# Performance work log

Hardware: AMD Instinct MI355X
Metric: run time of the kernel (lower is better)

Reference implementation:

```python
import jax, jax.numpy as jnp
import numpy as np

BS, C, H, W = 16, 64, 128, 128
NC = 80          # num classes (hardcoded 80 in original via expand(-1, 80, -1))
TOPK = 128
TAU = 0.07
EPS = 1e-12      # F.normalize eps


def setup_inputs() -> dict:
    key = jax.random.key(0)
    k1, k2, k3, k4 = jax.random.split(key, 4)
    feat = jax.random.normal(k1, (BS, C, H, W), dtype=jnp.float32)
    score = jax.random.uniform(k2, (BS, NC, H, W), dtype=jnp.float32)
    # hm: GT heatmap with exactly one 1.0 peak per (batch, class) for ~half the classes
    pos = jax.random.randint(k3, (BS, NC), 0, H * W)
    present = jax.random.bernoulli(k4, 0.5, (BS, NC)).astype(jnp.float32)
    b = jnp.arange(BS)[:, None]
    c = jnp.arange(NC)[None, :]
    hm = jnp.zeros((BS, NC, H * W), jnp.float32).at[b, c, pos].set(present)
    hm = hm.reshape(BS, NC, H, W)
    return {"feat": feat, "score": score, "hm": hm}


def reference(feat, score, hm):
    bs, c, h, w = feat.shape
    nc = hm.shape[1]
    hw = h * w
    score = jax.lax.stop_gradient(score)  # score.detach()

    # F.normalize(feat, dim=1)
    feat = feat / jnp.maximum(jnp.linalg.norm(feat, axis=1, keepdims=True), EPS)

    # q: feature at the hm==1 peak of each present class (one peak per (b,cls))
    peak = (hm == 1.0).astype(feat.dtype)                       # [bs,nc,h,w]
    q = jnp.einsum('bnhw,bchw->bnc', peak, feat)                # [bs,nc,c]
    class_mask = (peak.sum(axis=(2, 3)) > 0).astype(feat.dtype)  # [bs,nc]

    # k0: hm-weighted pooled feature per class, L2-normalized
    k0 = jnp.einsum('bchw,bnhw->bnc', feat, hm)                 # [bs,nc,c]
    k0 = k0 / jnp.maximum(jnp.linalg.norm(k0, axis=-1, keepdims=True), EPS)

    # mask score: zero at GT locations and for absent classes
    hm_free = (hm.sum(axis=1) == 0).astype(score.dtype)         # [bs,h,w]
    score = score * hm_free[:, None] * class_mask[:, :, None, None]

    max_values = score.max(axis=1).reshape(bs, hw)              # [bs,hw]
    class_indices = score.argmax(axis=1).reshape(bs, hw)        # [bs,hw]
    topk_values, topk_indices = jax.lax.top_k(max_values, TOPK)  # [bs,topk]
    k_all_mask_t = (topk_values > 0).astype(feat.dtype)         # [bs,topk]
    topk_class = jnp.take_along_axis(class_indices, topk_indices, axis=1)  # [bs,topk]

    feat_flat = feat.reshape(bs, c, hw)
    k_top = jnp.take_along_axis(feat_flat, topk_indices[:, None, :], axis=2)  # [bs,c,topk]
    k_top = k_top.transpose(0, 2, 1)                            # [bs,topk,c]

    # pseudo heatmap: 0.9 at selected (class, pos) pairs with positive score
    b_idx = jnp.arange(bs)[:, None]
    pseudo_hm = jnp.zeros((bs, nc, hw), feat.dtype).at[
        b_idx, topk_class, topk_indices].set(k_all_mask_t * 0.9)
    pseudo_hm = pseudo_hm.reshape(bs, nc, h, w)

    # positive mask: selected positions whose pseudo class matches the query class
    class_ids = jnp.arange(nc, dtype=feat.dtype)
    target = jnp.where(class_mask[:, :, None] == 1, class_ids[None, :, None], -1.0)  # [bs,nc,1]
    k_mask_top = (target == topk_class[:, None, :].astype(feat.dtype)).astype(feat.dtype)
    k_mask_top = k_mask_top * k_all_mask_t[:, None, :]          # [bs,nc,topk]
    k0_mask = class_mask[:, :, None] * jnp.eye(nc, dtype=feat.dtype)  # [bs,nc,nc]

    k_all = jnp.concatenate([k_top, k0], axis=1)                # [bs,topk+nc,c]
    k_mask = jnp.concatenate([k_mask_top, k0_mask], axis=-1)    # [bs,nc,topk+nc]
    k_all_mask = jnp.concatenate([k_all_mask_t, class_mask], axis=-1)  # [bs,topk+nc]

    sim = jnp.exp(jnp.einsum('bnc,bkc->bnk', q, k_all) / TAU)   # [bs,nc,topk+nc]
    sim_sum = (sim * k_all_mask[:, None, :]).sum(-1, keepdims=True)
    sim_sum = jnp.where(sim_sum == 0, 1.0, sim_sum)
    logit = jnp.where(k_mask > 0, sim / sim_sum, 1.0)
    log_loss = (jnp.log(logit) * k_mask).sum(-1)                # [bs,nc]
    num = k_mask.sum(-1)
    num = jnp.where(num == 0, 1.0, num)
    count = class_mask.sum()
    loss = ((log_loss / num) * class_mask).sum() / count
    return (-loss, pseudo_hm)
```

## Files before the change

### kernel.cpp

```cpp
#include <hip/hip_runtime.h>
#include <math.h>

#define BS 16
#define C 64
#define H 128
#define W 128
#define HW (H*W)
#define NC 80
#define TOPK 128
#define KALL (TOPK+NC)
#define TAU 0.07f
#define EPSN 1e-12f
#define OUT_N 20971521
#define ZBLK 1280

__global__ __launch_bounds__(1024) void k_peak_zero(const float* __restrict__ hm,
                                                    int* __restrict__ peak_pos,
                                                    float* __restrict__ out) {
    int t = threadIdx.x;
    if (blockIdx.x >= BS * NC) {
        int zb = blockIdx.x - BS * NC;
        float4* o4 = (float4*)out;
        float4 z = make_float4(0.f, 0.f, 0.f, 0.f);
        int idx = zb * 1024 + t;
        #pragma unroll
        for (int j = 0; j < 4; ++j) o4[idx + j * (ZBLK * 1024)] = z;
        if (zb == 0 && t == 0) out[OUT_N - 1] = 0.0f;
        return;
    }
    __shared__ int wmax[16];
    int bn = blockIdx.x;
    int lane = t & 63, wid = t >> 6;
    const float4* p = (const float4*)(hm + (size_t)bn * HW);
    int found = -1;
    #pragma unroll
    for (int j = 0; j < 4; ++j) {
        int gi = j * 1024 + t;
        float4 v = p[gi];
        int base = gi * 4;
        if (v.x == 1.0f) found = base;
        if (v.y == 1.0f) found = base + 1;
        if (v.z == 1.0f) found = base + 2;
        if (v.w == 1.0f) found = base + 3;
    }
    #pragma unroll
    for (int off = 1; off < 64; off <<= 1) found = max(found, __shfl_xor(found, off));
    if (lane == 0) wmax[wid] = found;
    __syncthreads();
    if (t == 0) {
        int m = wmax[0];
        #pragma unroll
        for (int i = 1; i < 16; ++i) m = max(m, wmax[i]);
        peak_pos[bn] = m;
    }
}

__global__ void k_max(const float* __restrict__ score, const int* __restrict__ peak_pos,
                      float* __restrict__ maxv, int* __restrict__ clsidx) {
    __shared__ int pk[NC];
    int b = blockIdx.y;
    int g = blockIdx.x * blockDim.x + threadIdx.x;
    if (threadIdx.x < NC) pk[threadIdx.x] = peak_pos[b * NC + threadIdx.x];
    __syncthreads();
    const float4* sb = (const float4*)(score + (size_t)b * NC * HW);
    int p0 = g * 4;
    int pp0 = pk[0];
    float m0 = (pp0 >= 0) ? 1.0f : 0.0f;
    float4 v0 = sb[g];
    float bx = v0.x * m0, by = v0.y * m0, bz = v0.z * m0, bw = v0.w * m0;
    int ix = 0, iy = 0, iz = 0, iw = 0;
    bool pe0 = (pp0 == p0), pe1 = (pp0 == p0 + 1), pe2 = (pp0 == p0 + 2), pe3 = (pp0 == p0 + 3);
    #pragma unroll 8
    for (int n = 1; n < NC; ++n) {
        int pp = pk[n];
        float m = (pp >= 0) ? 1.0f : 0.0f;
        float4 v = sb[(size_t)n * (HW / 4) + g];
        float vx = v.x * m, vy = v.y * m, vz = v.z * m, vw = v.w * m;
        if (vx > bx) { bx = vx; ix = n; }
        if (vy > by) { by = vy; iy = n; }
        if (vz > bz) { bz = vz; iz = n; }
        if (vw > bw) { bw = vw; iw = n; }
        pe0 |= (pp == p0); pe1 |= (pp == p0 + 1); pe2 |= (pp == p0 + 2); pe3 |= (pp == p0 + 3);
    }
    if (pe0) { bx = 0.0f; ix = 0; }
    if (pe1) { by = 0.0f; iy = 0; }
    if (pe2) { bz = 0.0f; iz = 0; }
    if (pe3) { bw = 0.0f; iw = 0; }
    ((float4*)maxv)[(size_t)b * (HW / 4) + g] = make_float4(bx, by, bz, bw);
    ((int4*)clsidx)[(size_t)b * (HW / 4) + g] = make_int4(ix, iy, iz, iw);
}

__global__ __launch_bounds__(1024) void k_topk(const float* __restrict__ maxv,
                                               const int* __restrict__ clsidx,
                                               float* __restrict__ topkv,
                                               int* __restrict__ topki,
                                               int* __restrict__ topkc) {
    __shared__ unsigned int hist[2048];
    __shared__ unsigned int wtot[16];
    __shared__ unsigned int woff[16];
    __shared__ unsigned int s_pref;
    __shared__ int s_rank;
    __shared__ unsigned int s_bin;
    __shared__ unsigned int s_above;

    int b = blockIdx.x, t = threadIdx.x;
    int lane = t & 63, wid = t >> 6;
    unsigned int key[16];
    const float4* mv4 = (const float4*)(maxv + (size_t)b * HW);
    #pragma unroll
    for (int j4 = 0; j4 < 4; ++j4) {
        float4 v = mv4[t * 4 + j4];
        key[j4 * 4 + 0] = __float_as_uint(v.x);
        key[j4 * 4 + 1] = __float_as_uint(v.y);
        key[j4 * 4 + 2] = __float_as_uint(v.z);
        key[j4 * 4 + 3] = __float_as_uint(v.w);
    }

    if (t == 0) { s_pref = 0u; s_rank = TOPK; }

    const int shifts[3] = {21, 10, 0};
    const int widths[3] = {11, 11, 10};

    for (int rnd = 0; rnd < 3; ++rnd) {
        int sh = shifts[rnd], w = widths[rnd];
        unsigned mask = (1u << w) - 1u;
        hist[t] = 0u; hist[t + 1024] = 0u;
        __syncthreads();
        unsigned pref = s_pref;
        int hiShift = sh + w;
        #pragma unroll
        for (int j = 0; j < 16; ++j) {
            unsigned k = key[j];
            bool ok = (rnd == 0) || ((k >> hiShift) == pref);
            if (ok) atomicAdd(&hist[(k >> sh) & mask], 1u);
        }
        __syncthreads();
        unsigned p = hist[2 * t] + hist[2 * t + 1];
        unsigned s = p;
        #pragma unroll
        for (int off = 1; off < 64; off <<= 1) {
            unsigned o = __shfl_down(s, off);
            if (lane + off < 64) s += o;
        }
        if (lane == 0) wtot[wid] = s;
        __syncthreads();
        if (wid == 0) {
            unsigned vv = (lane < 16) ? wtot[lane] : 0u;
            unsigned ss = vv;
            #pragma unroll
            for (int off = 1; off < 64; off <<= 1) {
                unsigned o = __shfl_down(ss, off);
                if (lane + off < 64) ss += o;
            }
            if (lane < 16) woff[lane] = ss - vv;
        }
        __syncthreads();
        unsigned S_t = s + woff[wid];
        unsigned S_next = S_t - p;
        int r = s_rank;
        if ((int)S_t >= r && (int)S_next < r) {
            unsigned hi = hist[2 * t + 1];
            if ((int)(S_next + hi) >= r) { s_bin = 2u * t + 1u; s_above = S_next; }
            else                         { s_bin = 2u * t;      s_above = S_next + hi; }
        }
        __syncthreads();
        if (t == 0) {
            s_pref = (s_pref << w) | s_bin;
            s_rank = s_rank - (int)s_above;
        }
        __syncthreads();
    }
    unsigned K = s_pref;
    int need_eq = s_rank;
    int cnt_gt = TOPK - need_eq;

    int cg = 0, ce = 0;
    #pragma unroll
    for (int j = 0; j < 16; ++j) { cg += (key[j] > K); ce += (key[j] == K); }
    unsigned v = ((unsigned)cg << 16) | (unsigned)ce;
    unsigned sc = v;
    #pragma unroll
    for (int off = 1; off < 64; off <<= 1) {
        unsigned o = __shfl_up(sc, off);
        if (lane >= off) sc += o;
    }
    if (lane == 63) wtot[wid] = sc;
    __syncthreads();
    if (wid == 0) {
        unsigned vv = (lane < 16) ? wtot[lane] : 0u;
        unsigned ss = vv;
        #pragma unroll
        for (int off = 1; off < 64; off <<= 1) {
            unsigned o = __shfl_up(ss, off);
            if (lane >= off) ss += o;
        }
        if (lane < 16) woff[lane] = ss - vv;
    }
    __syncthreads();
    unsigned ex = (sc - v) + woff[wid];
    int pg = (int)(ex >> 16);
    int pe = (int)(ex & 0xffffu);
    int lg = 0, le = 0;
    #pragma unroll
    for (int j = 0; j < 16; ++j) {
        unsigned k = key[j];
        int slot = -1;
        if (k > K) { slot = pg + lg; ++lg; }
        else if (k == K) { int er = pe + le; ++le; if (er < need_eq) slot = cnt_gt + er; }
        if (slot >= 0) {
            int idx = t * 16 + j;
            topkv[b * TOPK + slot] = __uint_as_float(k);
            topki[b * TOPK + slot] = idx;
            topkc[b * TOPK + slot] = clsidx[(size_t)b * HW + idx];
        }
    }
}

__global__ void k_gather(const float* __restrict__ feat, const int* __restrict__ peak_pos,
                         const int* __restrict__ topki, float* k_all, float* qv) {
    int bk = blockIdx.x;
    int b = bk / KALL, k = bk % KALL, c = threadIdx.x;
    int pos;
    if (k < TOPK) {
        pos = topki[b * TOPK + k];
    } else {
        int n = k - TOPK;
        int pp = peak_pos[b * NC + n];
        if (pp < 0) {
            k_all[((size_t)b * KALL + k) * C + c] = 0.0f;
            qv[((size_t)b * NC + n) * C + c] = 0.0f;
            return;
        }
        pos = pp;
    }
    float v = feat[((size_t)b * C + c) * HW + pos];
    float ss = v * v;
    #pragma unroll
    for (int off = 1; off < 64; off <<= 1) ss += __shfl_xor(ss, off);
    float qc = v / fmaxf(sqrtf(ss), EPSN);
    if (k < TOPK) {
        k_all[((size_t)b * KALL + k) * C + c] = qc;
    } else {
        int n = k - TOPK;
        qv[((size_t)b * NC + n) * C + c] = qc;
        float qq = qc * qc;
        #pragma unroll
        for (int off = 1; off < 64; off <<= 1) qq += __shfl_xor(qq, off);
        k_all[((size_t)b * KALL + k) * C + c] = qc / fmaxf(sqrtf(qq), EPSN);
    }
}

__global__ void k_loss(const float* __restrict__ k_all, const float* __restrict__ qv,
                       const int* __restrict__ peak_pos, const float* __restrict__ topkv,
                       const int* __restrict__ topkc, float* loss_bn) {
    __shared__ float qs[C];
    __shared__ float r1[256];
    __shared__ float r2[256];
    __shared__ float s_simsum, s_num;
    int bn = blockIdx.x;
    int b = bn / NC, n = bn % NC, t = threadIdx.x;
    if (peak_pos[bn] < 0) { if (t == 0) loss_bn[bn] = 0.0f; return; }
    if (t < C) qs[t] = qv[(size_t)bn * C + t];
    __syncthreads();
    float sim = 0.0f, kam = 0.0f, km = 0.0f;
    if (t < KALL) {
        const float* kr = k_all + ((size_t)b * KALL + t) * C;
        float dot = 0.0f;
        for (int c2 = 0; c2 < C; ++c2) dot += qs[c2] * kr[c2];
        sim = expf(dot / TAU);
        if (t < TOPK) {
            float posm = (topkv[b * TOPK + t] > 0.0f) ? 1.0f : 0.0f;
            kam = posm;
            km = (topkc[b * TOPK + t] == n) ? posm : 0.0f;
        } else {
            int j = t - TOPK;
            kam = (peak_pos[b * NC + j] >= 0) ? 1.0f : 0.0f;
            km = (j == n) ? 1.0f : 0.0f;
        }
    }
    r1[t] = sim * kam;
    r2[t] = km;
    __syncthreads();
    for (int s = 128; s > 0; s >>= 1) {
        if (t < s) { r1[t] += r1[t + s]; r2[t] += r2[t + s]; }
        __syncthreads();
    }
    if (t == 0) {
        float ss = r1[0];
        s_simsum = (ss == 0.0f) ? 1.0f : ss;
        s_num = (r2[0] == 0.0f) ? 1.0f : r2[0];
    }
    __syncthreads();
    r1[t] = (km > 0.0f) ? logf(sim / s_simsum) : 0.0f;
    __syncthreads();
    for (int s = 128; s > 0; s >>= 1) {
        if (t < s) r1[t] += r1[t + s];
        __syncthreads();
    }
    if (t == 0) loss_bn[bn] = r1[0] / s_num;
}

__global__ void k_scatter_final(const float* __restrict__ topkv, const int* __restrict__ topki,
                                const int* __restrict__ topkc,
                                const float* __restrict__ loss_bn,
                                const int* __restrict__ peak_pos, float* out) {
    if (blockIdx.x < 8) {
        int i = blockIdx.x * 256 + threadIdx.x;
        int b = i / TOPK;
        if (topkv[i] > 0.0f)
            out[1 + ((size_t)b * NC + topkc[i]) * HW + topki[i]] = 0.9f;
        return;
    }
    __shared__ float r1[256];
    __shared__ float r2[256];
    int t = threadIdx.x;
    float s = 0.0f, cnt = 0.0f;
    for (int i = t; i < BS * NC; i += 256) {
        s += loss_bn[i];
        cnt += (peak_pos[i] >= 0) ? 1.0f : 0.0f;
    }
    r1[t] = s; r2[t] = cnt;
    __syncthreads();
    for (int st = 128; st > 0; st >>= 1) {
        if (t < st) { r1[t] += r1[t + st]; r2[t] += r2[t + st]; }
        __syncthreads();
    }
    if (t == 0) out[0] = -(r1[0] / r2[0]);
}

extern "C" void kernel_launch(void* const* d_in, const int* in_sizes, int n_in,
                              void* d_out, int out_size, void* d_ws, size_t ws_size,
                              hipStream_t stream) {
    const float* feat  = (const float*)d_in[0];
    const float* score = (const float*)d_in[1];
    const float* hm    = (const float*)d_in[2];
    float* out = (float*)d_out;

    char* ws = (char*)d_ws;
    size_t off = 0;
    auto alloc = [&](size_t bytes) -> void* {
        void* p = ws + off;
        off += (bytes + 255) & ~(size_t)255;
        return p;
    };
    int*   peak_pos = (int*)  alloc((size_t)BS * NC * 4);
    float* maxv     = (float*)alloc((size_t)BS * HW * 4);
    int*   clsidx   = (int*)  alloc((size_t)BS * HW * 4);
    float* topkv    = (float*)alloc((size_t)BS * TOPK * 4);
    int*   topki    = (int*)  alloc((size_t)BS * TOPK * 4);
    int*   topkc    = (int*)  alloc((size_t)BS * TOPK * 4);
    float* k_all    = (float*)alloc((size_t)BS * KALL * C * 4);
    float* qv       = (float*)alloc((size_t)BS * NC * C * 4);
    float* loss_bn  = (float*)alloc((size_t)BS * NC * 4);

    k_peak_zero<<<BS * NC + ZBLK, 1024, 0, stream>>>(hm, peak_pos, out);
    dim3 gmax(HW / 4 / 256, BS);
    k_max<<<gmax, 256, 0, stream>>>(score, peak_pos, maxv, clsidx);
    k_topk<<<BS, 1024, 0, stream>>>(maxv, clsidx, topkv, topki, topkc);
    k_gather<<<BS * KALL, 64, 0, stream>>>(feat, peak_pos, topki, k_all, qv);
    k_loss<<<BS * NC, 256, 0, stream>>>(k_all, qv, peak_pos, topkv, topkc, loss_bn);
    k_scatter_final<<<9, 256, 0, stream>>>(topkv, topki, topkc, loss_bn, peak_pos, out);
}
```

Baseline: 93.48 us.

## Split output zeroing across first three kernels and fuse scatter into gather

The zero-fill of the large pseudo-heatmap output is split into three chunks. Extra blocks carrying those chunks are appended to the peak, max and top-k kernels, so the memset overlaps with the underutilized top-k and peak phases instead of running all at once in the first kernel. The 0.9 scatter moves into an extra block of the gather kernel, which now packs four rows per 256-thread block. The final reduction becomes a single-block kernel. This relies on the scatter running after all zeroing, which stream order still guarantees.

```diff
diff --git a/kernel.cpp b/kernel.cpp
--- a/kernel.cpp
+++ b/kernel.cpp
@@ -12,30 +12,32 @@
 #define TAU 0.07f
 #define EPSN 1e-12f
 #define OUT_N 20971521
-#define ZBLK 1280
-
-__global__ __launch_bounds__(1024) void k_peak_zero(const float* __restrict__ hm,
-                                                    int* __restrict__ peak_pos,
-                                                    float* __restrict__ out) {
+#define GBLK (BS*KALL/4)
+#define Z1BLK 1024
+#define Z2BLK 1024
+#define Z3BLK 256
+
+__global__ __launch_bounds__(256) void k_peak_z(const float* __restrict__ hm,
+                                                int* __restrict__ peak_pos,
+                                                float* __restrict__ out) {
     int t = threadIdx.x;
     if (blockIdx.x >= BS * NC) {
         int zb = blockIdx.x - BS * NC;
         float4* o4 = (float4*)out;
         float4 z = make_float4(0.f, 0.f, 0.f, 0.f);
-        int idx = zb * 1024 + t;
-        #pragma unroll
-        for (int j = 0; j < 4; ++j) o4[idx + j * (ZBLK * 1024)] = z;
-        if (zb == 0 && t == 0) out[OUT_N - 1] = 0.0f;
+        int base = zb * 2048;
+        #pragma unroll
+        for (int j = 0; j < 8; ++j) o4[base + j * 256 + t] = z;
         return;
     }
-    __shared__ int wmax[16];
+    __shared__ int wmax[4];
     int bn = blockIdx.x;
     int lane = t & 63, wid = t >> 6;
     const float4* p = (const float4*)(hm + (size_t)bn * HW);
     int found = -1;
     #pragma unroll
-    for (int j = 0; j < 4; ++j) {
-        int gi = j * 1024 + t;
+    for (int j = 0; j < 16; ++j) {
+        int gi = j * 256 + t;
         float4 v = p[gi];
         int base = gi * 4;
         if (v.x == 1.0f) found = base;
@@ -48,19 +50,30 @@
     if (lane == 0) wmax[wid] = found;
     __syncthreads();
     if (t == 0) {
-        int m = wmax[0];
-        #pragma unroll
-        for (int i = 1; i < 16; ++i) m = max(m, wmax[i]);
+        int m = max(max(wmax[0], wmax[1]), max(wmax[2], wmax[3]));
         peak_pos[bn] = m;
     }
 }
 
-__global__ void k_max(const float* __restrict__ score, const int* __restrict__ peak_pos,
-                      float* __restrict__ maxv, int* __restrict__ clsidx) {
+__global__ __launch_bounds__(256) void k_max_z(const float* __restrict__ score,
+                                               const int* __restrict__ peak_pos,
+                                               float* __restrict__ maxv,
+                                               int* __restrict__ clsidx,
+                                               float* __restrict__ out) {
+    int t = threadIdx.x;
+    if (blockIdx.x >= 256) {
+        int zb = blockIdx.x - 256;
+        float4* o4 = (float4*)out;
+        float4 z = make_float4(0.f, 0.f, 0.f, 0.f);
+        int base = 2097152 + zb * 2048;
+        #pragma unroll
+        for (int j = 0; j < 8; ++j) o4[base + j * 256 + t] = z;
+        return;
+    }
     __shared__ int pk[NC];
-    int b = blockIdx.y;
-    int g = blockIdx.x * blockDim.x + threadIdx.x;
-    if (threadIdx.x < NC) pk[threadIdx.x] = peak_pos[b * NC + threadIdx.x];
+    int b = blockIdx.x >> 4;
+    int g = (blockIdx.x & 15) * 256 + t;
+    if (t < NC) pk[t] = peak_pos[b * NC + t];
     __syncthreads();
     const float4* sb = (const float4*)(score + (size_t)b * NC * HW);
     int p0 = g * 4;
@@ -90,11 +103,23 @@
     ((int4*)clsidx)[(size_t)b * (HW / 4) + g] = make_int4(ix, iy, iz, iw);
 }
 
-__global__ __launch_bounds__(1024) void k_topk(const float* __restrict__ maxv,
-                                               const int* __restrict__ clsidx,
-                                               float* __restrict__ topkv,
-                                               int* __restrict__ topki,
-                                               int* __restrict__ topkc) {
+__global__ __launch_bounds__(1024) void k_topk_z(const float* __restrict__ maxv,
+                                                 const int* __restrict__ clsidx,
+                                                 float* __restrict__ topkv,
+                                                 int* __restrict__ topki,
+                                                 int* __restrict__ topkc,
+                                                 float* __restrict__ out) {
+    int t = threadIdx.x;
+    if (blockIdx.x >= BS) {
+        int zb = blockIdx.x - BS;
+        float4* o4 = (float4*)out;
+        float4 z = make_float4(0.f, 0.f, 0.f, 0.f);
+        int base = 4194304 + zb * 4096;
+        #pragma unroll
+        for (int j = 0; j < 4; ++j) o4[base + j * 1024 + t] = z;
+        if (zb == 0 && t == 0) out[OUT_N - 1] = 0.0f;
+        return;
+    }
     __shared__ unsigned int hist[2048];
     __shared__ unsigned int wtot[16];
     __shared__ unsigned int woff[16];
@@ -103,8 +128,9 @@
     __shared__ unsigned int s_bin;
     __shared__ unsigned int s_above;
 
-    int b = blockIdx.x, t = threadIdx.x;
+    int b = blockIdx.x;
     int lane = t & 63, wid = t >> 6;
+
     unsigned int key[16];
     const float4* mv4 = (const float4*)(maxv + (size_t)b * HW);
     #pragma unroll
@@ -216,10 +242,29 @@
     }
 }
 
-__global__ void k_gather(const float* __restrict__ feat, const int* __restrict__ peak_pos,
-                         const int* __restrict__ topki, float* k_all, float* qv) {
-    int bk = blockIdx.x;
-    int b = bk / KALL, k = bk % KALL, c = threadIdx.x;
+__global__ __launch_bounds__(256) void k_gather_sc(const float* __restrict__ feat,
+                                                   const int* __restrict__ peak_pos,
+                                                   const float* __restrict__ topkv,
+                                                   const int* __restrict__ topki,
+                                                   const int* __restrict__ topkc,
+                                                   float* __restrict__ k_all,
+                                                   float* __restrict__ qv,
+                                                   float* __restrict__ out) {
+    int t = threadIdx.x;
+    if (blockIdx.x == GBLK) {
+        #pragma unroll
+        for (int j = 0; j < 8; ++j) {
+            int i = j * 256 + t;
+            if (topkv[i] > 0.0f) {
+                int b = i >> 7;
+                out[1 + (((size_t)b * NC + topkc[i]) << 14) + topki[i]] = 0.9f;
+            }
+        }
+        return;
+    }
+    int wid = t >> 6, lane = t & 63;
+    int bk = blockIdx.x * 4 + wid;
+    int b = bk / KALL, k = bk % KALL, c = lane;
     int pos;
     if (k < TOPK) {
         pos = topki[b * TOPK + k];
@@ -250,9 +295,12 @@
     }
 }
 
-__global__ void k_loss(const float* __restrict__ k_all, const float* __restrict__ qv,
-                       const int* __restrict__ peak_pos, const float* __restrict__ topkv,
-                       const int* __restrict__ topkc, float* loss_bn) {
+__global__ __launch_bounds__(256) void k_loss(const float* __restrict__ k_all,
+                                              const float* __restrict__ qv,
+                                              const int* __restrict__ peak_pos,
+                                              const float* __restrict__ topkv,
+                                              const int* __restrict__ topkc,
+                                              float* __restrict__ loss_bn) {
     __shared__ float qs[C];
     __shared__ float r1[256];
     __shared__ float r2[256];
@@ -300,17 +348,9 @@
     if (t == 0) loss_bn[bn] = r1[0] / s_num;
 }
 
-__global__ void k_scatter_final(const float* __restrict__ topkv, const int* __restrict__ topki,
-                                const int* __restrict__ topkc,
-                                const float* __restrict__ loss_bn,
-                                const int* __restrict__ peak_pos, float* out) {
-    if (blockIdx.x < 8) {
-        int i = blockIdx.x * 256 + threadIdx.x;
-        int b = i / TOPK;
-        if (topkv[i] > 0.0f)
-            out[1 + ((size_t)b * NC + topkc[i]) * HW + topki[i]] = 0.9f;
-        return;
-    }
+__global__ __launch_bounds__(256) void k_final(const float* __restrict__ loss_bn,
+                                               const int* __restrict__ peak_pos,
+                                               float* __restrict__ out) {
     __shared__ float r1[256];
     __shared__ float r2[256];
     int t = threadIdx.x;
@@ -353,11 +393,11 @@
     float* qv       = (float*)alloc((size_t)BS * NC * C * 4);
     float* loss_bn  = (float*)alloc((size_t)BS * NC * 4);
 
-    k_peak_zero<<<BS * NC + ZBLK, 1024, 0, stream>>>(hm, peak_pos, out);
-    dim3 gmax(HW / 4 / 256, BS);
-    k_max<<<gmax, 256, 0, stream>>>(score, peak_pos, maxv, clsidx);
-    k_topk<<<BS, 1024, 0, stream>>>(maxv, clsidx, topkv, topki, topkc);
-    k_gather<<<BS * KALL, 64, 0, stream>>>(feat, peak_pos, topki, k_all, qv);
+    k_peak_z<<<BS * NC + Z1BLK, 256, 0, stream>>>(hm, peak_pos, out);
+    k_max_z<<<256 + Z2BLK, 256, 0, stream>>>(score, peak_pos, maxv, clsidx, out);
+    k_topk_z<<<BS + Z3BLK, 1024, 0, stream>>>(maxv, clsidx, topkv, topki, topkc, out);
+    k_gather_sc<<<GBLK + 1, 256, 0, stream>>>(feat, peak_pos, topkv, topki, topkc,
+                                              k_all, qv, out);
     k_loss<<<BS * NC, 256, 0, stream>>>(k_all, qv, peak_pos, topkv, topkc, loss_bn);
-    k_scatter_final<<<9, 256, 0, stream>>>(topkv, topki, topkc, loss_bn, peak_pos, out);
-}
+    k_final<<<1, 256, 0, stream>>>(loss_bn, peak_pos, out);
+}
```

After: 100.2 us. 1.07x slower.

## Fuse scatter into gather and final reduction into loss via last-block counter

Applied to the files above, without the earlier changes.

Moves the pseudo-heatmap scatter into an extra block of the gather kernel, which now packs four 64-lane gathers per 256-thread block. The final loss reduction is folded into the loss kernel: each block fences, bumps a global counter, and the last block to arrive does the global sum. The counter is reset inside the topk kernel. This drops one kernel launch and its dependency gap, at the cost of an atomic and a threadfence in every loss block.

```diff
diff --git a/kernel.cpp b/kernel.cpp
--- a/kernel.cpp
+++ b/kernel.cpp
@@ -13,6 +13,8 @@
 #define EPSN 1e-12f
 #define OUT_N 20971521
 #define ZBLK 1280
+#define GBLK (BS*KALL/4)
+#define LOSSBLK (BS*NC)
 
 __global__ __launch_bounds__(1024) void k_peak_zero(const float* __restrict__ hm,
                                                     int* __restrict__ peak_pos,
@@ -94,7 +96,8 @@
                                                const int* __restrict__ clsidx,
                                                float* __restrict__ topkv,
                                                int* __restrict__ topki,
-                                               int* __restrict__ topkc) {
+                                               int* __restrict__ topkc,
+                                               int* __restrict__ counter) {
     __shared__ unsigned int hist[2048];
     __shared__ unsigned int wtot[16];
     __shared__ unsigned int woff[16];
@@ -105,6 +108,8 @@
 
     int b = blockIdx.x, t = threadIdx.x;
     int lane = t & 63, wid = t >> 6;
+    if (b == 0 && t == 0) *counter = 0;
+
     unsigned int key[16];
     const float4* mv4 = (const float4*)(maxv + (size_t)b * HW);
     #pragma unroll
@@ -216,10 +221,29 @@
     }
 }
 
-__global__ void k_gather(const float* __restrict__ feat, const int* __restrict__ peak_pos,
-                         const int* __restrict__ topki, float* k_all, float* qv) {
-    int bk = blockIdx.x;
-    int b = bk / KALL, k = bk % KALL, c = threadIdx.x;
+__global__ __launch_bounds__(256) void k_gather_sc(const float* __restrict__ feat,
+                                                   const int* __restrict__ peak_pos,
+                                                   const float* __restrict__ topkv,
+                                                   const int* __restrict__ topki,
+                                                   const int* __restrict__ topkc,
+                                                   float* __restrict__ k_all,
+                                                   float* __restrict__ qv,
+                                                   float* __restrict__ out) {
+    int t = threadIdx.x;
+    if (blockIdx.x == GBLK) {
+        #pragma unroll
+        for (int j = 0; j < 8; ++j) {
+            int i = j * 256 + t;
+            if (topkv[i] > 0.0f) {
+                int b = i >> 7;
+                out[1 + (((size_t)b * NC + topkc[i]) << 14) + topki[i]] = 0.9f;
+            }
+        }
+        return;
+    }
+    int wid = t >> 6, lane = t & 63;
+    int bk = blockIdx.x * 4 + wid;
+    int b = bk / KALL, k = bk % KALL, c = lane;
     int pos;
     if (k < TOPK) {
         pos = topki[b * TOPK + k];
@@ -250,82 +274,84 @@
     }
 }
 
-__global__ void k_loss(const float* __restrict__ k_all, const float* __restrict__ qv,
-                       const int* __restrict__ peak_pos, const float* __restrict__ topkv,
-                       const int* __restrict__ topkc, float* loss_bn) {
+__global__ __launch_bounds__(256) void k_loss_final(const float* __restrict__ k_all,
+                                                    const float* __restrict__ qv,
+                                                    const int* __restrict__ peak_pos,
+                                                    const float* __restrict__ topkv,
+                                                    const int* __restrict__ topkc,
+                                                    float* __restrict__ loss_bn,
+                                                    int* __restrict__ counter,
+                                                    float* __restrict__ out) {
     __shared__ float qs[C];
     __shared__ float r1[256];
     __shared__ float r2[256];
     __shared__ float s_simsum, s_num;
+    __shared__ int s_last;
     int bn = blockIdx.x;
     int b = bn / NC, n = bn % NC, t = threadIdx.x;
-    if (peak_pos[bn] < 0) { if (t == 0) loss_bn[bn] = 0.0f; return; }
-    if (t < C) qs[t] = qv[(size_t)bn * C + t];
-    __syncthreads();
+    bool present = (peak_pos[bn] >= 0);
     float sim = 0.0f, kam = 0.0f, km = 0.0f;
-    if (t < KALL) {
-        const float* kr = k_all + ((size_t)b * KALL + t) * C;
-        float dot = 0.0f;
-        for (int c2 = 0; c2 < C; ++c2) dot += qs[c2] * kr[c2];
-        sim = expf(dot / TAU);
-        if (t < TOPK) {
-            float posm = (topkv[b * TOPK + t] > 0.0f) ? 1.0f : 0.0f;
-            kam = posm;
-            km = (topkc[b * TOPK + t] == n) ? posm : 0.0f;
-        } else {
-            int j = t - TOPK;
-            kam = (peak_pos[b * NC + j] >= 0) ? 1.0f : 0.0f;
-            km = (j == n) ? 1.0f : 0.0f;
-        }
-    }
-    r1[t] = sim * kam;
-    r2[t] = km;
-    __syncthreads();
-    for (int s = 128; s > 0; s >>= 1) {
-        if (t < s) { r1[t] += r1[t + s]; r2[t] += r2[t + s]; }
-        __syncthreads();
-    }
-    if (t == 0) {
-        float ss = r1[0];
-        s_simsum = (ss == 0.0f) ? 1.0f : ss;
-        s_num = (r2[0] == 0.0f) ? 1.0f : r2[0];
-    }
-    __syncthreads();
-    r1[t] = (km > 0.0f) ? logf(sim / s_simsum) : 0.0f;
-    __syncthreads();
-    for (int s = 128; s > 0; s >>= 1) {
-        if (t < s) r1[t] += r1[t + s];
-        __syncthreads();
-    }
-    if (t == 0) loss_bn[bn] = r1[0] / s_num;
-}
-
-__global__ void k_scatter_final(const float* __restrict__ topkv, const int* __restrict__ topki,
-                                const int* __restrict__ topkc,
-                                const float* __restrict__ loss_bn,
-                                const int* __restrict__ peak_pos, float* out) {
-    if (blockIdx.x < 8) {
-        int i = blockIdx.x * 256 + threadIdx.x;
-        int b = i / TOPK;
-        if (topkv[i] > 0.0f)
-            out[1 + ((size_t)b * NC + topkc[i]) * HW + topki[i]] = 0.9f;
-        return;
-    }
-    __shared__ float r1[256];
-    __shared__ float r2[256];
-    int t = threadIdx.x;
-    float s = 0.0f, cnt = 0.0f;
-    for (int i = t; i < BS * NC; i += 256) {
-        s += loss_bn[i];
-        cnt += (peak_pos[i] >= 0) ? 1.0f : 0.0f;
-    }
-    r1[t] = s; r2[t] = cnt;
-    __syncthreads();
-    for (int st = 128; st > 0; st >>= 1) {
-        if (t < st) { r1[t] += r1[t + st]; r2[t] += r2[t + st]; }
-        __syncthreads();
-    }
-    if (t == 0) out[0] = -(r1[0] / r2[0]);
+    if (present) {
+        if (t < C) qs[t] = qv[(size_t)bn * C + t];
+        __syncthreads();
+        if (t < KALL) {
+            const float* kr = k_all + ((size_t)b * KALL + t) * C;
+            float dot = 0.0f;
+            for (int c2 = 0; c2 < C; ++c2) dot += qs[c2] * kr[c2];
+            sim = expf(dot / TAU);
+            if (t < TOPK) {
+                float posm = (topkv[b * TOPK + t] > 0.0f) ? 1.0f : 0.0f;
+                kam = posm;
+                km = (topkc[b * TOPK + t] == n) ? posm : 0.0f;
+            } else {
+                int j = t - TOPK;
+                kam = (peak_pos[b * NC + j] >= 0) ? 1.0f : 0.0f;
+                km = (j == n) ? 1.0f : 0.0f;
+            }
+        }
+        r1[t] = sim * kam;
+        r2[t] = km;
+        __syncthreads();
+        for (int s = 128; s > 0; s >>= 1) {
+            if (t < s) { r1[t] += r1[t + s]; r2[t] += r2[t + s]; }
+            __syncthreads();
+        }
+        if (t == 0) {
+            float ss = r1[0];
+            s_simsum = (ss == 0.0f) ? 1.0f : ss;
+            s_num = (r2[0] == 0.0f) ? 1.0f : r2[0];
+        }
+        __syncthreads();
+        r1[t] = (km > 0.0f) ? logf(sim / s_simsum) : 0.0f;
+        __syncthreads();
+        for (int s = 128; s > 0; s >>= 1) {
+            if (t < s) r1[t] += r1[t + s];
+            __syncthreads();
+        }
+        if (t == 0) loss_bn[bn] = r1[0] / s_num;
+    } else {
+        if (t == 0) loss_bn[bn] = 0.0f;
+        __syncthreads();
+    }
+    __threadfence();
+    __syncthreads();
+    if (t == 0) s_last = (atomicAdd(counter, 1) == LOSSBLK - 1) ? 1 : 0;
+    __syncthreads();
+    if (s_last) {
+        __threadfence();
+        float s = 0.0f, cnt = 0.0f;
+        for (int i = t; i < BS * NC; i += 256) {
+            s += loss_bn[i];
+            cnt += (peak_pos[i] >= 0) ? 1.0f : 0.0f;
+        }
+        r1[t] = s; r2[t] = cnt;
+        __syncthreads();
+        for (int st = 128; st > 0; st >>= 1) {
+            if (t < st) { r1[t] += r1[t + st]; r2[t] += r2[t + st]; }
+            __syncthreads();
+        }
+        if (t == 0) out[0] = -(r1[0] / r2[0]);
+    }
 }
 
 extern "C" void kernel_launch(void* const* d_in, const int* in_sizes, int n_in,
@@ -352,12 +378,14 @@
     float* k_all    = (float*)alloc((size_t)BS * KALL * C * 4);
     float* qv       = (float*)alloc((size_t)BS * NC * C * 4);
     float* loss_bn  = (float*)alloc((size_t)BS * NC * 4);
+    int*   counter  = (int*)  alloc(256);
 
     k_peak_zero<<<BS * NC + ZBLK, 1024, 0, stream>>>(hm, peak_pos, out);
     dim3 gmax(HW / 4 / 256, BS);
     k_max<<<gmax, 256, 0, stream>>>(score, peak_pos, maxv, clsidx);
-    k_topk<<<BS, 1024, 0, stream>>>(maxv, clsidx, topkv, topki, topkc);
-    k_gather<<<BS * KALL, 64, 0, stream>>>(feat, peak_pos, topki, k_all, qv);
-    k_loss<<<BS * NC, 256, 0, stream>>>(k_all, qv, peak_pos, topkv, topkc, loss_bn);
-    k_scatter_final<<<9, 256, 0, stream>>>(topkv, topki, topkc, loss_bn, peak_pos, out);
-}
+    k_topk<<<BS, 1024, 0, stream>>>(maxv, clsidx, topkv, topki, topkc, counter);
+    k_gather_sc<<<GBLK + 1, 256, 0, stream>>>(feat, peak_pos, topkv, topki, topkc,
+                                              k_all, qv, out);
+    k_loss_final<<<LOSSBLK, 256, 0, stream>>>(k_all, qv, peak_pos, topkv, topkc,
+                                              loss_bn, counter, out);
+}
```

Result: slower. 186.2 us (+99.2%).
